# Optimization experiments

Hardware: AMD Instinct MI355X
Metric: run time of the kernel (lower is better)

Reference implementation:

```python
import jax, jax.numpy as jnp
import numpy as np

B, N, F_IN, OUT = 1, 8192, 256, 64

def setup_inputs() -> dict:
    key = jax.random.key(0)
    k1, k2, k3, k4 = jax.random.split(key, 4)
    seq = jax.random.normal(k1, (B, N, F_IN), dtype=jnp.float32)
    bias_mat = jnp.zeros((B, N, N), dtype=jnp.float32)  # 0 = fully connected; -1e9 entries mask edges
    W1 = jax.random.normal(k2, (F_IN, OUT), dtype=jnp.float32) * 0.05
    a1 = jax.random.normal(k3, (OUT, 1), dtype=jnp.float32) * 0.05
    b1 = jnp.zeros((1,), dtype=jnp.float32)
    a2 = jax.random.normal(k4, (OUT, 1), dtype=jnp.float32) * 0.05
    b2 = jnp.zeros((1,), dtype=jnp.float32)
    return {"seq": seq, "bias_mat": bias_mat, "W1": W1, "a1": a1, "b1": b1, "a2": a2, "b2": b2}

def reference(seq, bias_mat, W1, a1, b1, a2, b2):
    # Conv1D(kernel=1) == matmul over the feature dim
    seq_fts = jnp.einsum('bnf,fo->bno', seq, W1)          # [B,N,OUT]
    f_1 = jnp.einsum('bno,ok->bnk', seq_fts, a1) + b1      # [B,N,1]
    f_2 = jnp.einsum('bno,ok->bnk', seq_fts, a2) + b2      # [B,N,1]
    logits = f_1 + jnp.swapaxes(f_2, 1, 2)                  # [B,N,N] additive outer-sum
    coefs = jax.nn.softmax(jax.nn.leaky_relu(logits, negative_slope=0.2) + bias_mat, axis=-1)
    vals = jnp.einsum('bnm,bmo->bno', coefs, seq_fts)       # [B,N,OUT]
    return jax.nn.elu(vals)
```

## Files before the change

kernel.cpp:

```cpp
#include <hip/hip_runtime.h>
#include <hip/hip_bf16.h>


typedef float f32x4 __attribute__((ext_vector_type(4)));
typedef short bf16x8 __attribute__((ext_vector_type(8)));

__device__ __forceinline__ unsigned short f2bf(float x) {
    union { float f; unsigned u; } v; v.f = x;
    unsigned r = v.u + 0x7FFF + ((v.u >> 16) & 1);
    return (unsigned short)(r >> 16);
}

__device__ __forceinline__ float elu1(float x) {
    return x > 0.f ? x : (__expf(x) - 1.f);
}

__device__ __forceinline__ void gld_lds16(const void* g, void* l) {
    __builtin_amdgcn_global_load_lds(
        (const __attribute__((address_space(1))) void*)(unsigned long long)g,
        (__attribute__((address_space(3))) void*)(unsigned)(unsigned long long)l,
        16, 0, 0);
}

__global__ __launch_bounds__(256) void attn_fts(
    const float* __restrict__ seq, const float* __restrict__ W1,
    const float* __restrict__ a1, const float* __restrict__ b1,
    const float* __restrict__ a2, const float* __restrict__ b2,
    unsigned short* __restrict__ ftsT, float* __restrict__ f1g,
    float* __restrict__ f2g)
{
    __shared__ unsigned short w1t[64 * 264];
    __shared__ unsigned short stage[64 * 40];
    __shared__ float f1p[2][32];
    __shared__ float f2p[2][32];

    const int tid = threadIdx.x;
    const int qb = blockIdx.x * 32;
    const int w = tid >> 6, rg = w & 1, oh = w >> 1;
    const int lane = tid & 63, c = lane & 15, g = lane >> 4;

    for (int i = 0; i < 64; ++i) {
        int e = tid + i * 256;
        int k = e >> 6, o = e & 63;
        w1t[o * 264 + k] = f2bf(W1[e]);
    }
    __syncthreads();

    f32x4 acc[2] = {};
    const float* srow = seq + (long)(qb + rg * 16 + c) * 256;
    #pragma unroll
    for (int ks = 0; ks < 8; ++ks) {
        int k0 = ks * 32 + g * 8;
        float4 s0 = *(const float4*)(srow + k0);
        float4 s1 = *(const float4*)(srow + k0 + 4);
        bf16x8 af;
        af[0] = (short)f2bf(s0.x); af[1] = (short)f2bf(s0.y);
        af[2] = (short)f2bf(s0.z); af[3] = (short)f2bf(s0.w);
        af[4] = (short)f2bf(s1.x); af[5] = (short)f2bf(s1.y);
        af[6] = (short)f2bf(s1.z); af[7] = (short)f2bf(s1.w);
        #pragma unroll
        for (int ob = 0; ob < 2; ++ob) {
            int brow = oh * 32 + ob * 16 + c;
            bf16x8 bf = *(const bf16x8*)(&w1t[brow * 264 + k0]);
            acc[ob] = __builtin_amdgcn_mfma_f32_16x16x32_bf16(af, bf, acc[ob], 0, 0, 0);
        }
    }

    float a1v0 = a1[oh * 32 + c], a1v1 = a1[oh * 32 + 16 + c];
    float a2v0 = a2[oh * 32 + c], a2v1 = a2[oh * 32 + 16 + c];
    #pragma unroll
    for (int reg = 0; reg < 4; ++reg) {
        float p1 = acc[0][reg] * a1v0 + acc[1][reg] * a1v1;
        float p2 = acc[0][reg] * a2v0 + acc[1][reg] * a2v1;
        #pragma unroll
        for (int mm = 1; mm < 16; mm <<= 1) {
            p1 += __shfl_xor(p1, mm, 64);
            p2 += __shfl_xor(p2, mm, 64);
        }
        if (c == 0) {
            f1p[oh][rg * 16 + g * 4 + reg] = p1;
            f2p[oh][rg * 16 + g * 4 + reg] = p2;
        }
    }

    #pragma unroll
    for (int ob = 0; ob < 2; ++ob) {
        int row = oh * 32 + ob * 16 + c;
        #pragma unroll
        for (int rp = 0; rp < 2; ++rp) {
            unsigned short lo = f2bf(acc[ob][rp * 2]);
            unsigned short hi = f2bf(acc[ob][rp * 2 + 1]);
            unsigned v = (unsigned)lo | ((unsigned)hi << 16);
            *(unsigned*)(&stage[row * 40 + rg * 16 + g * 4 + rp * 2]) = v;
        }
    }
    __syncthreads();

    {
        int o = tid >> 2, q4 = tid & 3;
        uint4 v = *(const uint4*)(&stage[o * 40 + q4 * 8]);
        *(uint4*)(&ftsT[(long)o * 8192 + qb + q4 * 8]) = v;
    }
    if (tid < 32) {
        f1g[qb + tid] = f1p[0][tid] + f1p[1][tid] + b1[0];
        f2g[qb + tid] = f2p[0][tid] + f2p[1][tid] + b2[0];
    }
}

__global__ __launch_bounds__(256) void attn_main(
    const float* __restrict__ bias, const unsigned short* __restrict__ ftsT,
    const float* __restrict__ f1g, const float* __restrict__ f2g,
    float* __restrict__ out)
{
    __shared__ float blds[2][16][260];
    __shared__ float macc[4][16][68];
    __shared__ float mlm[4][16];
    __shared__ float mll[4][16];

    const int tid = threadIdx.x;
    const int qb = blockIdx.x * 16;
    const int h = tid >> 6;
    const int lane = tid & 63, c = lane & 15, g = lane >> 4;

    const float f1r = f1g[qb + c];

    float m = -INFINITY, lsum = 0.f;
    f32x4 acc[4] = {};

    auto issue_round = [&](int r, int buf) {
        #pragma unroll
        for (int i = 0; i < 4; ++i) {
            const int row = h * 4 + i;
            const float* gsrc = bias + (long)(qb + row) * 8192 + r * 256 + lane * 4;
            gld_lds16(gsrc, &blds[buf][row][0]);
        }
    };

    auto do_ks = [&](int r, int ks) {
        const int jcol = h * 64 + ks * 32 + g * 8;
        const float* bl = &blds[r & 1][c][jcol];
        float4 b0 = *(const float4*)(bl);
        float4 b1v = *(const float4*)(bl + 4);
        const int jg = r * 256 + jcol;
        const unsigned short* fp = ftsT + (long)c * 8192 + jg;
        bf16x8 ff0 = *(const bf16x8*)(fp);
        bf16x8 ff1 = *(const bf16x8*)(fp + 16 * 8192);
        bf16x8 ff2 = *(const bf16x8*)(fp + 32 * 8192);
        bf16x8 ff3 = *(const bf16x8*)(fp + 48 * 8192);
        const float* qp = f2g + jg;
        float4 fa = ((const float4*)qp)[0];
        float4 fb = ((const float4*)qp)[1];

        float bb[8] = { b0.x, b0.y, b0.z, b0.w, b1v.x, b1v.y, b1v.z, b1v.w };
        float f2v[8] = { fa.x, fa.y, fa.z, fa.w, fb.x, fb.y, fb.z, fb.w };
        float s[8];
        float tm = -INFINITY;
        #pragma unroll
        for (int i = 0; i < 8; ++i) {
            float z = f1r + f2v[i];
            z = fmaxf(z, 0.2f * z);
            float sv = z + bb[i];
            s[i] = sv;
            tm = fmaxf(tm, sv);
        }
        tm = fmaxf(tm, __shfl_xor(tm, 16, 64));
        tm = fmaxf(tm, __shfl_xor(tm, 32, 64));
        if (!__all(tm <= m + 8.f)) {
            float mnew = fmaxf(m, tm);
            float sc = __expf(m - mnew);
            lsum *= sc;
            float scq0 = __shfl(sc, g * 4 + 0, 64);
            float scq1 = __shfl(sc, g * 4 + 1, 64);
            float scq2 = __shfl(sc, g * 4 + 2, 64);
            float scq3 = __shfl(sc, g * 4 + 3, 64);
            #pragma unroll
            for (int ob = 0; ob < 4; ++ob) {
                acc[ob][0] *= scq0; acc[ob][1] *= scq1;
                acc[ob][2] *= scq2; acc[ob][3] *= scq3;
            }
            m = mnew;
        }
        float ts = 0.f;
        bf16x8 af;
        #pragma unroll
        for (int i = 0; i < 8; ++i) {
            float p = __expf(s[i] - m);
            ts += p;
            af[i] = (short)f2bf(p);
        }
        ts += __shfl_xor(ts, 16, 64);
        ts += __shfl_xor(ts, 32, 64);
        lsum += ts;
        acc[0] = __builtin_amdgcn_mfma_f32_16x16x32_bf16(af, ff0, acc[0], 0, 0, 0);
        acc[1] = __builtin_amdgcn_mfma_f32_16x16x32_bf16(af, ff1, acc[1], 0, 0, 0);
        acc[2] = __builtin_amdgcn_mfma_f32_16x16x32_bf16(af, ff2, acc[2], 0, 0, 0);
        acc[3] = __builtin_amdgcn_mfma_f32_16x16x32_bf16(af, ff3, acc[3], 0, 0, 0);
    };

    issue_round(0, 0);
    #pragma unroll 1
    for (int r = 0; r < 32; ++r) {
        __syncthreads();
        if (r + 1 < 32) issue_round(r + 1, (r + 1) & 1);
        do_ks(r, 0);
        do_ks(r, 1);
    }

    __syncthreads();
    #pragma unroll
    for (int ob = 0; ob < 4; ++ob) {
        macc[h][g * 4 + 0][ob * 16 + c] = acc[ob][0];
        macc[h][g * 4 + 1][ob * 16 + c] = acc[ob][1];
        macc[h][g * 4 + 2][ob * 16 + c] = acc[ob][2];
        macc[h][g * 4 + 3][ob * 16 + c] = acc[ob][3];
    }
    if (lane < 16) { mlm[h][c] = m; mll[h][c] = lsum; }
    __syncthreads();

    {
        const int row = tid >> 4;
        const int o0 = (tid & 15) * 4;
        float m0 = mlm[0][row], m1 = mlm[1][row];
        float m2 = mlm[2][row], m3 = mlm[3][row];
        float ms = fmaxf(fmaxf(m0, m1), fmaxf(m2, m3));
        float w0 = __expf(m0 - ms), w1 = __expf(m1 - ms);
        float w2 = __expf(m2 - ms), w3 = __expf(m3 - ms);
        float den = mll[0][row] * w0 + mll[1][row] * w1 +
                    mll[2][row] * w2 + mll[3][row] * w3;
        float inv = 1.f / den;
        float4 v0 = *(const float4*)(&macc[0][row][o0]);
        float4 v1 = *(const float4*)(&macc[1][row][o0]);
        float4 v2 = *(const float4*)(&macc[2][row][o0]);
        float4 v3 = *(const float4*)(&macc[3][row][o0]);
        float4 res;
        res.x = elu1((v0.x * w0 + v1.x * w1 + v2.x * w2 + v3.x * w3) * inv);
        res.y = elu1((v0.y * w0 + v1.y * w1 + v2.y * w2 + v3.y * w3) * inv);
        res.z = elu1((v0.z * w0 + v1.z * w1 + v2.z * w2 + v3.z * w3) * inv);
        res.w = elu1((v0.w * w0 + v1.w * w1 + v2.w * w2 + v3.w * w3) * inv);
        *(float4*)(&out[(long)(qb + row) * 64 + o0]) = res;
    }
}

extern "C" void kernel_launch(void* const* d_in, const int* in_sizes, int n_in,
                              void* d_out, int out_size, void* d_ws, size_t ws_size,
                              hipStream_t stream) {
    (void)in_sizes; (void)n_in; (void)out_size; (void)ws_size;
    const float* seq  = (const float*)d_in[0];
    const float* bias = (const float*)d_in[1];
    const float* W1   = (const float*)d_in[2];
    const float* a1   = (const float*)d_in[3];
    const float* b1   = (const float*)d_in[4];
    const float* a2   = (const float*)d_in[5];
    const float* b2   = (const float*)d_in[6];
    float* out = (float*)d_out;

    unsigned short* ftsT = (unsigned short*)d_ws;
    float* f1 = (float*)((char*)d_ws + 64 * 8192 * 2);
    float* f2 = (float*)((char*)d_ws + 64 * 8192 * 2 + 8192 * 4);

    hipLaunchKernelGGL(attn_fts, dim3(256), dim3(256), 0, stream,
                       seq, W1, a1, b1, a2, b2, ftsT, f1, f2);
    hipLaunchKernelGGL(attn_main, dim3(512), dim3(256), 0, stream,
                       bias, ftsT, f1, f2, out);
}
```

Measured before the change: 395.8 us.

## Deepen attention main loop pipeline with register-prefetched features and 4-stage bias ring

Restructures the main attention loop into a manually unrolled two-round ping-pong. Feature and f2 loads for the next round are prefetched into registers, and the bias tiles stream through a 4-deep LDS ring with explicit vmcnt waits and raw barriers in place of __syncthreads. The epilogue reduction buffers now alias the bias LDS, and launch bounds request 2 blocks per SM. This is meant to hide global-load latency behind the MFMA work, at the cost of higher register and LDS pressure and fragile hand-counted waitcnt ordering.

```diff
diff --git a/kernel.cpp b/kernel.cpp
--- a/kernel.cpp
+++ b/kernel.cpp
@@ -4,6 +4,11 @@
 
 typedef float f32x4 __attribute__((ext_vector_type(4)));
 typedef short bf16x8 __attribute__((ext_vector_type(8)));
+
+#define WAITCNT4() asm volatile("s_waitcnt vmcnt(4)" ::: "memory")
+#define WAITCNT0() asm volatile("s_waitcnt vmcnt(0)" ::: "memory")
+#define SBAR() __builtin_amdgcn_s_barrier()
+#define SCHEDB() __builtin_amdgcn_sched_barrier(0)
 
 __device__ __forceinline__ unsigned short f2bf(float x) {
     union { float f; unsigned u; } v; v.f = x;
@@ -107,15 +112,12 @@
     }
 }
 
-__global__ __launch_bounds__(256) void attn_main(
+__global__ __launch_bounds__(256, 2) void attn_main(
     const float* __restrict__ bias, const unsigned short* __restrict__ ftsT,
     const float* __restrict__ f1g, const float* __restrict__ f2g,
     float* __restrict__ out)
 {
-    __shared__ float blds[2][16][260];
-    __shared__ float macc[4][16][68];
-    __shared__ float mlm[4][16];
-    __shared__ float mll[4][16];
+    __shared__ float blds[4][16][260];
 
     const int tid = threadIdx.x;
     const int qb = blockIdx.x * 16;
@@ -127,7 +129,8 @@
     float m = -INFINITY, lsum = 0.f;
     f32x4 acc[4] = {};
 
-    auto issue_round = [&](int r, int buf) {
+    auto issue_bias = [&](int r) {
+        const int buf = r & 3;
         #pragma unroll
         for (int i = 0; i < 4; ++i) {
             const int row = h * 4 + i;
@@ -136,21 +139,46 @@
         }
     };
 
-    auto do_ks = [&](int r, int ks) {
+    bf16x8 A00, A01, A02, A03, A10, A11, A12, A13;
+    float4 Af0, Af1, Af2, Af3;
+    bf16x8 B00, B01, B02, B03, B10, B11, B12, B13;
+    float4 Bf0, Bf1, Bf2, Bf3;
+
+    auto loadF_A = [&](int r) {
+        const unsigned short* p = ftsT + (long)c * 8192 + r * 256 + h * 64 + g * 8;
+        A00 = *(const bf16x8*)(p);
+        A01 = *(const bf16x8*)(p + 16 * 8192);
+        A02 = *(const bf16x8*)(p + 32 * 8192);
+        A03 = *(const bf16x8*)(p + 48 * 8192);
+        A10 = *(const bf16x8*)(p + 32);
+        A11 = *(const bf16x8*)(p + 32 + 16 * 8192);
+        A12 = *(const bf16x8*)(p + 32 + 32 * 8192);
+        A13 = *(const bf16x8*)(p + 32 + 48 * 8192);
+        const float* q = f2g + r * 256 + h * 64 + g * 8;
+        Af0 = ((const float4*)q)[0]; Af1 = ((const float4*)q)[1];
+        Af2 = ((const float4*)(q + 32))[0]; Af3 = ((const float4*)(q + 32))[1];
+    };
+    auto loadF_B = [&](int r) {
+        const unsigned short* p = ftsT + (long)c * 8192 + r * 256 + h * 64 + g * 8;
+        B00 = *(const bf16x8*)(p);
+        B01 = *(const bf16x8*)(p + 16 * 8192);
+        B02 = *(const bf16x8*)(p + 32 * 8192);
+        B03 = *(const bf16x8*)(p + 48 * 8192);
+        B10 = *(const bf16x8*)(p + 32);
+        B11 = *(const bf16x8*)(p + 32 + 16 * 8192);
+        B12 = *(const bf16x8*)(p + 32 + 32 * 8192);
+        B13 = *(const bf16x8*)(p + 32 + 48 * 8192);
+        const float* q = f2g + r * 256 + h * 64 + g * 8;
+        Bf0 = ((const float4*)q)[0]; Bf1 = ((const float4*)q)[1];
+        Bf2 = ((const float4*)(q + 32))[0]; Bf3 = ((const float4*)(q + 32))[1];
+    };
+
+    auto do_ks = [&](int r, int ks, bf16x8 ff0, bf16x8 ff1, bf16x8 ff2,
+                     bf16x8 ff3, float4 fa, float4 fb) {
         const int jcol = h * 64 + ks * 32 + g * 8;
-        const float* bl = &blds[r & 1][c][jcol];
+        const float* bl = &blds[r & 3][c][jcol];
         float4 b0 = *(const float4*)(bl);
         float4 b1v = *(const float4*)(bl + 4);
-        const int jg = r * 256 + jcol;
-        const unsigned short* fp = ftsT + (long)c * 8192 + jg;
-        bf16x8 ff0 = *(const bf16x8*)(fp);
-        bf16x8 ff1 = *(const bf16x8*)(fp + 16 * 8192);
-        bf16x8 ff2 = *(const bf16x8*)(fp + 32 * 8192);
-        bf16x8 ff3 = *(const bf16x8*)(fp + 48 * 8192);
-        const float* qp = f2g + jg;
-        float4 fa = ((const float4*)qp)[0];
-        float4 fb = ((const float4*)qp)[1];
-
         float bb[8] = { b0.x, b0.y, b0.z, b0.w, b1v.x, b1v.y, b1v.z, b1v.w };
         float f2v[8] = { fa.x, fa.y, fa.z, fa.w, fb.x, fb.y, fb.z, fb.w };
         float s[8];
@@ -197,16 +225,44 @@
         acc[3] = __builtin_amdgcn_mfma_f32_16x16x32_bf16(af, ff3, acc[3], 0, 0, 0);
     };
 
-    issue_round(0, 0);
+    loadF_A(0);
+    SCHEDB();
+    issue_bias(0);
+    issue_bias(1);
+
     #pragma unroll 1
-    for (int r = 0; r < 32; ++r) {
-        __syncthreads();
-        if (r + 1 < 32) issue_round(r + 1, (r + 1) & 1);
-        do_ks(r, 0);
-        do_ks(r, 1);
-    }
+    for (int rp = 0; rp < 15; ++rp) {
+        const int r = 2 * rp;
+        WAITCNT4(); SBAR(); SCHEDB();
+        loadF_B(r + 1);
+        SCHEDB();
+        issue_bias(r + 2);
+        SCHEDB();
+        do_ks(r, 0, A00, A01, A02, A03, Af0, Af1);
+        do_ks(r, 1, A10, A11, A12, A13, Af2, Af3);
+
+        WAITCNT4(); SBAR(); SCHEDB();
+        loadF_A(r + 2);
+        SCHEDB();
+        issue_bias(r + 3);
+        SCHEDB();
+        do_ks(r + 1, 0, B00, B01, B02, B03, Bf0, Bf1);
+        do_ks(r + 1, 1, B10, B11, B12, B13, Bf2, Bf3);
+    }
+    WAITCNT4(); SBAR(); SCHEDB();
+    loadF_B(31);
+    SCHEDB();
+    do_ks(30, 0, A00, A01, A02, A03, Af0, Af1);
+    do_ks(30, 1, A10, A11, A12, A13, Af2, Af3);
+    WAITCNT0(); SBAR(); SCHEDB();
+    do_ks(31, 0, B00, B01, B02, B03, Bf0, Bf1);
+    do_ks(31, 1, B10, B11, B12, B13, Bf2, Bf3);
 
     __syncthreads();
+    float (*macc)[16][68] = (float (*)[16][68])(&blds[0][0][0]);
+    float* mlm = ((float*)macc) + 4 * 16 * 68;
+    float* mll = mlm + 64;
+
     #pragma unroll
     for (int ob = 0; ob < 4; ++ob) {
         macc[h][g * 4 + 0][ob * 16 + c] = acc[ob][0];
@@ -214,19 +270,19 @@
         macc[h][g * 4 + 2][ob * 16 + c] = acc[ob][2];
         macc[h][g * 4 + 3][ob * 16 + c] = acc[ob][3];
     }
-    if (lane < 16) { mlm[h][c] = m; mll[h][c] = lsum; }
+    if (lane < 16) { mlm[h * 16 + c] = m; mll[h * 16 + c] = lsum; }
     __syncthreads();
 
     {
         const int row = tid >> 4;
         const int o0 = (tid & 15) * 4;
-        float m0 = mlm[0][row], m1 = mlm[1][row];
-        float m2 = mlm[2][row], m3 = mlm[3][row];
+        float m0 = mlm[0 * 16 + row], m1 = mlm[1 * 16 + row];
+        float m2 = mlm[2 * 16 + row], m3 = mlm[3 * 16 + row];
         float ms = fmaxf(fmaxf(m0, m1), fmaxf(m2, m3));
         float w0 = __expf(m0 - ms), w1 = __expf(m1 - ms);
         float w2 = __expf(m2 - ms), w3 = __expf(m3 - ms);
-        float den = mll[0][row] * w0 + mll[1][row] * w1 +
-                    mll[2][row] * w2 + mll[3][row] * w3;
+        float den = mll[0 * 16 + row] * w0 + mll[1 * 16 + row] * w1 +
+                    mll[2 * 16 + row] * w2 + mll[3 * 16 + row] * w3;
         float inv = 1.f / den;
         float4 v0 = *(const float4*)(&macc[0][row][o0]);
         float4 v1 = *(const float4*)(&macc[1][row][o0]);
```

New measurement: 387.8 us. 2.0% less time.
